# Kernel tuning notes

Measured on AMD Instinct MI355X. Metric: run time of the kernel, lower is better.

Reference implementation:

```python
import jax, jax.numpy as jnp
import numpy as np

V, E, L = 32000, 512, 2  # vocab_size, n_embd (== hidden), n_layer
B, T = 8, 1024


def setup_inputs() -> dict:
    key = jax.random.key(0)
    ks = jax.random.split(key, 6)
    inp = jax.random.randint(ks[0], (B, T), 0, V)
    wte = jax.random.normal(ks[1], (V, E), dtype=jnp.float32) * 0.02
    # PyTorch LSTM params per layer: weight_ih [4H, in], weight_hh [4H, H], b_ih [4H], b_hh [4H]
    W_ih = jax.random.normal(ks[2], (L, 4 * E, E), dtype=jnp.float32) * 0.04
    W_hh = jax.random.normal(ks[3], (L, 4 * E, E), dtype=jnp.float32) * 0.04
    b_ih = jnp.zeros((L, 4 * E), dtype=jnp.float32)
    b_hh = jnp.zeros((L, 4 * E), dtype=jnp.float32)
    fc_w = jax.random.normal(ks[4], (V, E), dtype=jnp.float32) * 0.02
    fc_b = jnp.zeros((V,), dtype=jnp.float32)
    return {"inp": inp, "wte": wte, "W_ih": W_ih, "W_hh": W_hh,
            "b_ih": b_ih, "b_hh": b_hh, "fc_w": fc_w, "fc_b": fc_b}


def _lstm_stack(x, W_ih, W_hh, b_ih, b_hh):
    # x: [B, T, E]; multi-layer LSTM, zero initial (h, c), PyTorch gate order i,f,g,o
    H = W_hh.shape[-1]
    n_layers = W_ih.shape[0]
    for l in range(n_layers):
        # input-to-hidden part is time-parallel: precompute once per layer
        xg = jnp.einsum('bte,ge->btg', x, W_ih[l]) + b_ih[l] + b_hh[l]  # [B,T,4H]
        Whh = W_hh[l]
        h0 = jnp.zeros((x.shape[0], H), x.dtype)
        c0 = jnp.zeros((x.shape[0], H), x.dtype)

        def step(carry, xg_t, Whh=Whh):
            h, c = carry
            g = xg_t + h @ Whh.T  # [B,4H]
            i, f, gg, o = jnp.split(g, 4, axis=-1)
            c = jax.nn.sigmoid(f) * c + jax.nn.sigmoid(i) * jnp.tanh(gg)
            h = jax.nn.sigmoid(o) * jnp.tanh(c)
            return (h, c), h

        (_, _), hs = jax.lax.scan(step, (h0, c0), jnp.swapaxes(xg, 0, 1))  # hs: [T,B,H]
        x = jnp.swapaxes(hs, 0, 1)  # [B,T,H] feeds next layer
    return x


def reference(inp, wte, W_ih, W_hh, b_ih, b_hh, fc_w, fc_b):
    x = wte[inp]  # [B,T,E] embedding lookup
    h = _lstm_stack(x, W_ih, W_hh, b_ih, b_hh)  # [B,T,H]
    logits = jnp.einsum('bth,vh->btv', h, fc_w) + fc_b  # [B,T,V]
    return logits
```

## Files before the change

### kernel.cpp

```cpp
#include <hip/hip_runtime.h>
#include <stdint.h>

typedef __attribute__((ext_vector_type(4))) float f32x4;
typedef __attribute__((ext_vector_type(8))) short s16x8;
typedef __attribute__((ext_vector_type(4))) unsigned short u16x4;
typedef __attribute__((ext_vector_type(4))) unsigned int u32x4;

#define T_SEQ 1024
#define HID 512

__device__ __forceinline__ unsigned short f2bf(float f) {
  uint32_t u = __float_as_uint(f);
  u += 0x7fffu + ((u >> 16) & 1u);
  return (unsigned short)(u >> 16);
}
__device__ __forceinline__ float sigf(float x) { return 1.f / (1.f + __expf(-x)); }
__device__ __forceinline__ float tanhfast(float x) {
  float e = __expf(2.f * x);
  return (e - 1.f) / (e + 1.f);
}

#define ASTORE(p, v) __hip_atomic_store((p), (v), __ATOMIC_RELAXED, __HIP_MEMORY_SCOPE_AGENT)

__device__ __forceinline__ u32x4 load_coh16(const unsigned int* p) {
  u32x4 r;
  asm volatile("global_load_dwordx4 %0, %1, off sc0 sc1" : "=v"(r) : "v"(p) : "memory");
  return r;
}
#define VM_WAIT0 do { asm volatile("s_waitcnt vmcnt(0)" ::: "memory"); \
                      __builtin_amdgcn_sched_barrier(0); } while (0)

#define GLL(gp, lp)                                                      \
  __builtin_amdgcn_global_load_lds(                                     \
      (const __attribute__((address_space(1))) void*)(gp),              \
      (__attribute__((address_space(3))) void*)(lp), 16, 0, 0)

__global__ __launch_bounds__(256) void embed_kernel(const int* __restrict__ inp,
                                                    const float* __restrict__ wte,
                                                    unsigned short* __restrict__ xbf) {
  const int m = blockIdx.x;
  const int idx = inp[m];
  const float* src = wte + (size_t)idx * HID;
  unsigned short* dst = xbf + (size_t)m * HID;
  const int e = threadIdx.x;
  dst[e] = f2bf(src[e]);
  dst[e + 256] = f2bf(src[e + 256]);
}

__global__ __launch_bounds__(256) void cvt_bf16_kernel(const float* __restrict__ src,
                                                       unsigned short* __restrict__ dst,
                                                       int n4) {
  const int i = blockIdx.x * 256 + threadIdx.x;
  if (i >= n4) return;
  f32x4 v = ((const f32x4*)src)[i];
  u16x4 o;
  o.x = f2bf(v.x); o.y = f2bf(v.y); o.z = f2bf(v.z); o.w = f2bf(v.w);
  ((u16x4*)dst)[i] = o;
}

__global__ __launch_bounds__(256) void bias_sum_kernel(const float* __restrict__ a,
                                                       const float* __restrict__ b,
                                                       float* __restrict__ o, int n) {
  const int i = blockIdx.x * 256 + threadIdx.x;
  if (i < n) o[i] = a[i] + b[i];
}

template <int MODE>
__global__ __launch_bounds__(256) void gemm_bt(const unsigned short* __restrict__ A,
                                               const unsigned short* __restrict__ B,
                                               float* __restrict__ C,
                                               const float* __restrict__ bias,
                                               int M, int N, int K) {
  __shared__ unsigned short As[128 * 32];
  __shared__ unsigned short Bs[128 * 32];
  const int nTiles = N >> 7;
  const int mt = blockIdx.x / nTiles;
  const int nt = blockIdx.x - mt * nTiles;
  const int m0 = mt << 7, n0 = nt << 7;
  const int tid = threadIdx.x;
  const int wave = tid >> 6, lane = tid & 63;
  const int wm = wave >> 1, wn = wave & 1;

  const int c1 = wave * 64 + lane;
  const int c2 = 256 + c1;
  const unsigned short* gA1 = A + (size_t)(m0 + (c1 >> 2)) * K + (c1 & 3) * 8;
  const unsigned short* gA2 = A + (size_t)(m0 + (c2 >> 2)) * K + (c2 & 3) * 8;
  const unsigned short* gB1 = B + (size_t)(n0 + (c1 >> 2)) * K + (c1 & 3) * 8;
  const unsigned short* gB2 = B + (size_t)(n0 + (c2 >> 2)) * K + (c2 & 3) * 8;
  unsigned short* lA1 = As + wave * 512;
  unsigned short* lA2 = As + 2048 + wave * 512;
  unsigned short* lB1 = Bs + wave * 512;
  unsigned short* lB2 = Bs + 2048 + wave * 512;

  f32x4 acc[4][4] = {};
  const int row_lo = lane & 15;
  const int kq = (lane >> 4) * 8;

  for (int k0 = 0; k0 < K; k0 += 32) {
    GLL(gA1 + k0, lA1);
    GLL(gA2 + k0, lA2);
    GLL(gB1 + k0, lB1);
    GLL(gB2 + k0, lB2);
    __syncthreads();
    s16x8 af[4], bfr[4];
#pragma unroll
    for (int f = 0; f < 4; ++f) {
      af[f] = *(const s16x8*)(As + (wm * 64 + f * 16 + row_lo) * 32 + kq);
      bfr[f] = *(const s16x8*)(Bs + (wn * 64 + f * 16 + row_lo) * 32 + kq);
    }
#pragma unroll
    for (int i = 0; i < 4; ++i)
#pragma unroll
      for (int j = 0; j < 4; ++j)
        acc[i][j] = __builtin_amdgcn_mfma_f32_16x16x32_bf16(af[i], bfr[j], acc[i][j], 0, 0, 0);
    __syncthreads();
  }

  float bv[4];
#pragma unroll
  for (int j = 0; j < 4; ++j) bv[j] = bias[n0 + wn * 64 + j * 16 + row_lo];
  const int rbase = (lane >> 4) * 4;
#pragma unroll
  for (int i = 0; i < 4; ++i) {
#pragma unroll
    for (int r = 0; r < 4; ++r) {
      const int m = m0 + wm * 64 + i * 16 + rbase + r;
      const size_t row = MODE == 1 ? ((size_t)(m & 7) * T_SEQ + (m >> 3))
                       : MODE == 2 ? ((size_t)(m & (T_SEQ - 1)) * 8 + (m >> 10))
                                   : (size_t)m;
      float* cp = C + row * (size_t)N;
#pragma unroll
      for (int j = 0; j < 4; ++j) cp[n0 + wn * 64 + j * 16 + row_lo] = acc[i][j][r] + bv[j];
    }
  }
}

template <bool IS_L1>
__device__ __forceinline__ void lstm_side(
    int wg, int tid,
    const float* __restrict__ xg1t,
    const unsigned short* __restrict__ Wa,
    const unsigned short* __restrict__ Wb,
    const float* __restrict__ bias2,
    unsigned int* __restrict__ h1T,
    unsigned int* __restrict__ h2T,
    unsigned short* __restrict__ h2out,
    char* hlds, float* GT) {
  constexpr int NKT = IS_L1 ? 16 : 32;
  constexpr int RB = IS_L1 ? 1024 : 2048;
  const int g = tid >> 6, l = tid & 63;
  const int unit = l & 15, grp = l >> 4;
  const int u0 = wg * 16;
  const int row = l & 7;

  s16x8 bfr[NKT];
  {
    const size_t grow = (size_t)(g * 512 + u0 + unit) * 512;
#pragma unroll
    for (int kt = 0; kt < NKT; ++kt) {
      const unsigned short* W = (IS_L1 || kt < 16) ? Wa : Wb;
      bfr[kt] = *(const s16x8*)(W + grow + (kt & 15) * 32 + grp * 8);
    }
  }

  const int sr = tid & 7, sc = tid >> 3;
  const int sb0 = (sr * RB + sc * 32) ^ (sr << 4);
  const int sb1 = (sr * RB + sc * 32 + 16) ^ (sr << 4);
  const int sb2 = (sr * RB + 1024 + sc * 32) ^ (sr << 4);
  const int sb3 = (sr * RB + 1024 + sc * 32 + 16) ^ (sr << 4);

  const int pb = l & 7, pu = l >> 3;
  float bias_g[2][4];
  if constexpr (!IS_L1) {
    if (g == 0) {
#pragma unroll
      for (int r = 0; r < 2; ++r)
#pragma unroll
        for (int gg = 0; gg < 4; ++gg)
          bias_g[r][gg] = bias2[gg * 512 + u0 + r * 8 + pu];
    }
  }
  float cst0 = 0.f, cst1 = 0.f;

  for (int t = 0; t < T_SEQ; ++t) {
    float xv[2][4];
    if constexpr (IS_L1) {
      if (g == 0) {
#pragma unroll
        for (int r = 0; r < 2; ++r)
#pragma unroll
          for (int gg = 0; gg < 4; ++gg)
            xv[r][gg] = xg1t[(size_t)(t * 8 + pb) * 2048 + gg * 512 + u0 + r * 8 + pu];
      }
    }

    if constexpr (IS_L1) {
      u32x4 w0 = {}, w1 = {};
      if (t > 0) {
        const unsigned int* src = h1T + (size_t)(t - 1) * 4096 + sr * 512 + sc * 16;
        const unsigned int tg = (unsigned int)t;
        u32x4 d0, d1, d2, d3;
        for (;;) {
          d0 = load_coh16(src); d1 = load_coh16(src + 4);
          d2 = load_coh16(src + 8); d3 = load_coh16(src + 12);
          VM_WAIT0;
          bool ok = true;
#pragma unroll
          for (int j = 0; j < 4; ++j) {
            ok &= (d0[j] >> 16) == tg; ok &= (d1[j] >> 16) == tg;
            ok &= (d2[j] >> 16) == tg; ok &= (d3[j] >> 16) == tg;
          }
          if (__ballot(ok) == ~0ULL) break;
          __builtin_amdgcn_s_sleep(1);
        }
        w0 = u32x4{(d0[0] & 0xffffu) | (d0[1] << 16), (d0[2] & 0xffffu) | (d0[3] << 16),
                   (d1[0] & 0xffffu) | (d1[1] << 16), (d1[2] & 0xffffu) | (d1[3] << 16)};
        w1 = u32x4{(d2[0] & 0xffffu) | (d2[1] << 16), (d2[2] & 0xffffu) | (d2[3] << 16),
                   (d3[0] & 0xffffu) | (d3[1] << 16), (d3[2] & 0xffffu) | (d3[3] << 16)};
      }
      *(u32x4*)(hlds + sb0) = w0;
      *(u32x4*)(hlds + sb1) = w1;
    } else {
      const unsigned int* src1 = h1T + (size_t)t * 4096 + sr * 512 + sc * 16;
      const unsigned int tg1 = (unsigned int)(t + 1);
      u32x4 d0, d1, d2, d3, e0 = {}, e1 = {}, e2 = {}, e3 = {};
      if (t > 0) {
        const unsigned int* src2 = h2T + (size_t)(t - 1) * 4096 + sr * 512 + sc * 16;
        const unsigned int tg2 = (unsigned int)t;
        for (;;) {
          d0 = load_coh16(src1); d1 = load_coh16(src1 + 4);
          d2 = load_coh16(src1 + 8); d3 = load_coh16(src1 + 12);
          e0 = load_coh16(src2); e1 = load_coh16(src2 + 4);
          e2 = load_coh16(src2 + 8); e3 = load_coh16(src2 + 12);
          VM_WAIT0;
          bool ok = true;
#pragma unroll
          for (int j = 0; j < 4; ++j) {
            ok &= (d0[j] >> 16) == tg1; ok &= (d1[j] >> 16) == tg1;
            ok &= (d2[j] >> 16) == tg1; ok &= (d3[j] >> 16) == tg1;
            ok &= (e0[j] >> 16) == tg2; ok &= (e1[j] >> 16) == tg2;
            ok &= (e2[j] >> 16) == tg2; ok &= (e3[j] >> 16) == tg2;
          }
          if (__ballot(ok) == ~0ULL) break;
          __builtin_amdgcn_s_sleep(1);
        }
      } else {
        for (;;) {
          d0 = load_coh16(src1); d1 = load_coh16(src1 + 4);
          d2 = load_coh16(src1 + 8); d3 = load_coh16(src1 + 12);
          VM_WAIT0;
          bool ok = true;
#pragma unroll
          for (int j = 0; j < 4; ++j) {
            ok &= (d0[j] >> 16) == tg1; ok &= (d1[j] >> 16) == tg1;
            ok &= (d2[j] >> 16) == tg1; ok &= (d3[j] >> 16) == tg1;
          }
          if (__ballot(ok) == ~0ULL) break;
          __builtin_amdgcn_s_sleep(1);
        }
      }
      *(u32x4*)(hlds + sb0) =
          u32x4{(d0[0] & 0xffffu) | (d0[1] << 16), (d0[2] & 0xffffu) | (d0[3] << 16),
                (d1[0] & 0xffffu) | (d1[1] << 16), (d1[2] & 0xffffu) | (d1[3] << 16)};
      *(u32x4*)(hlds + sb1) =
          u32x4{(d2[0] & 0xffffu) | (d2[1] << 16), (d2[2] & 0xffffu) | (d2[3] << 16),
                (d3[0] & 0xffffu) | (d3[1] << 16), (d3[2] & 0xffffu) | (d3[3] << 16)};
      *(u32x4*)(hlds + sb2) =
          u32x4{(e0[0] & 0xffffu) | (e0[1] << 16), (e0[2] & 0xffffu) | (e0[3] << 16),
                (e1[0] & 0xffffu) | (e1[1] << 16), (e1[2] & 0xffffu) | (e1[3] << 16)};
      *(u32x4*)(hlds + sb3) =
          u32x4{(e2[0] & 0xffffu) | (e2[1] << 16), (e2[2] & 0xffffu) | (e2[3] << 16),
                (e3[0] & 0xffffu) | (e3[1] << 16), (e3[2] & 0xffffu) | (e3[3] << 16)};
    }
    __syncthreads();

    f32x4 a0 = {}, a1 = {}, a2 = {}, a3 = {};
#pragma unroll
    for (int kt = 0; kt < NKT; kt += 4) {
      s16x8 x0 = *(const s16x8*)(hlds + ((row * RB + (kt + 0) * 64 + grp * 16) ^ (row << 4)));
      s16x8 x1 = *(const s16x8*)(hlds + ((row * RB + (kt + 1) * 64 + grp * 16) ^ (row << 4)));
      s16x8 x2 = *(const s16x8*)(hlds + ((row * RB + (kt + 2) * 64 + grp * 16) ^ (row << 4)));
      s16x8 x3 = *(const s16x8*)(hlds + ((row * RB + (kt + 3) * 64 + grp * 16) ^ (row << 4)));
      a0 = __builtin_amdgcn_mfma_f32_16x16x32_bf16(x0, bfr[kt + 0], a0, 0, 0, 0);
      a1 = __builtin_amdgcn_mfma_f32_16x16x32_bf16(x1, bfr[kt + 1], a1, 0, 0, 0);
      a2 = __builtin_amdgcn_mfma_f32_16x16x32_bf16(x2, bfr[kt + 2], a2, 0, 0, 0);
      a3 = __builtin_amdgcn_mfma_f32_16x16x32_bf16(x3, bfr[kt + 3], a3, 0, 0, 0);
    }
    f32x4 acc = (a0 + a1) + (a2 + a3);

    if (grp < 2) *(f32x4*)(GT + g * 128 + unit * 8 + grp * 4) = acc;
    __syncthreads();

    if (g == 0) {
      const unsigned int tago = (unsigned int)(t + 1) << 16;
#pragma unroll
      for (int r = 0; r < 2; ++r) {
        const int u = r * 8 + pu;
        float gi = GT[0 + u * 8 + pb];
        float gf = GT[128 + u * 8 + pb];
        float gg = GT[256 + u * 8 + pb];
        float go = GT[384 + u * 8 + pb];
        if constexpr (IS_L1) {
          gi += xv[r][0]; gf += xv[r][1]; gg += xv[r][2]; go += xv[r][3];
        } else {
          gi += bias_g[r][0]; gf += bias_g[r][1]; gg += bias_g[r][2]; go += bias_g[r][3];
        }
        float& cc = r ? cst1 : cst0;
        cc = sigf(gf) * cc + sigf(gi) * tanhfast(gg);
        const float hv = sigf(go) * tanhfast(cc);
        const unsigned int hb16 = f2bf(hv);
        unsigned int* hT = IS_L1 ? h1T : h2T;
        ASTORE(hT + (size_t)t * 4096 + pb * 512 + u0 + u, hb16 | tago);
        if constexpr (!IS_L1)
          h2out[(size_t)(t * 8 + pb) * 512 + u0 + u] = (unsigned short)hb16;
      }
    }
  }
}

__global__ __launch_bounds__(256, 1) void lstm_kernel(
    const float* __restrict__ xg1t,
    const unsigned short* __restrict__ whh1,
    const unsigned short* __restrict__ wih2,
    const unsigned short* __restrict__ whh2,
    const float* __restrict__ bias2,
    unsigned int* __restrict__ h1T, unsigned int* __restrict__ h2T,
    unsigned short* __restrict__ h2out) {
  __shared__ __align__(16) char hlds[16384];
  __shared__ float GT[512];
  const int wg = blockIdx.x, tid = threadIdx.x;
  if (wg < 32)
    lstm_side<true>(wg, tid, xg1t, whh1, nullptr, nullptr, h1T, h2T, h2out, hlds, GT);
  else
    lstm_side<false>(wg - 32, tid, xg1t, wih2, whh2, bias2, h1T, h2T, h2out, hlds, GT);
}

extern "C" void kernel_launch(void* const* d_in, const int* in_sizes, int n_in,
                              void* d_out, int out_size, void* d_ws, size_t ws_size,
                              hipStream_t stream) {
  (void)in_sizes; (void)n_in; (void)out_size; (void)ws_size;
  const int* inp = (const int*)d_in[0];
  const float* wte = (const float*)d_in[1];
  const float* W_ih = (const float*)d_in[2];
  const float* W_hh = (const float*)d_in[3];
  const float* b_ih = (const float*)d_in[4];
  const float* b_hh = (const float*)d_in[5];
  const float* fc_w = (const float*)d_in[6];
  const float* fc_b = (const float*)d_in[7];
  float* out = (float*)d_out;

  char* ob = (char*)d_out;
  float* xg1t = (float*)(ob);
  unsigned int* h1T = (unsigned int*)(ob + (64u << 20));
  unsigned int* h2T = (unsigned int*)(ob + (80u << 20));
  unsigned short* x_bf = (unsigned short*)(ob + (96u << 20));
  unsigned short* whh_bf = (unsigned short*)(ob + (104u << 20));
  unsigned short* wih_bf = (unsigned short*)(ob + (108u << 20));

  char* ws = (char*)d_ws;
  unsigned short* fcw_bf = (unsigned short*)(ws);
  float* bias12 = (float*)(ws + (32u << 20));
  unsigned short* h2bf = (unsigned short*)(ws + (35u << 20));

  hipMemsetAsync(ob + (64u << 20), 0, 32u << 20, stream);
  embed_kernel<<<8192, 256, 0, stream>>>(inp, wte, x_bf);
  cvt_bf16_kernel<<<2048, 256, 0, stream>>>(W_ih, wih_bf, 2 * 2048 * 512 / 4);
  cvt_bf16_kernel<<<2048, 256, 0, stream>>>(W_hh, whh_bf, 2 * 2048 * 512 / 4);
  cvt_bf16_kernel<<<16000, 256, 0, stream>>>(fc_w, fcw_bf, 32000 * 512 / 4);
  bias_sum_kernel<<<16, 256, 0, stream>>>(b_ih, b_hh, bias12, 4096);
  gemm_bt<2><<<64 * 16, 256, 0, stream>>>(x_bf, wih_bf, xg1t, bias12, 8192, 2048, 512);
  lstm_kernel<<<64, 256, 0, stream>>>(xg1t, whh_bf, wih_bf + (size_t)2048 * 512,
                                      whh_bf + (size_t)2048 * 512, bias12 + 2048,
                                      h1T, h2T, h2bf);
  gemm_bt<1><<<64 * 250, 256, 0, stream>>>(h2bf, fcw_bf, out, fc_b, 8192, 32000, 512);
}
```

Baseline: 4.935 ms.

## Fuse both LSTM layers into one 32-workgroup wavefront-pipelined kernel

Replaces the split design, where 32 workgroups ran layer 1 and 32 ran layer 2, with one kernel in which each of 32 workgroups computes a 16-unit slice of both layers. Layer 2 runs two steps behind layer 1 and reads a double-buffered layer-1 hidden state. The xg1 GEMM output goes back to row-major order, so the transposed store mode is dropped. Each group now holds all three weight slices in registers and does more serial work per step. In exchange the per-step flag polls cover both layers in one loop, and the spin loop has a bounded iteration cap that could fall through without valid data.

```diff
diff --git a/kernel.cpp b/kernel.cpp
--- a/kernel.cpp
+++ b/kernel.cpp
@@ -21,6 +21,7 @@
 }
 
 #define ASTORE(p, v) __hip_atomic_store((p), (v), __ATOMIC_RELAXED, __HIP_MEMORY_SCOPE_AGENT)
+#define MFMA(a, b, c) __builtin_amdgcn_mfma_f32_16x16x32_bf16((a), (b), (c), 0, 0, 0)
 
 __device__ __forceinline__ u32x4 load_coh16(const unsigned int* p) {
   u32x4 r;
@@ -112,7 +113,7 @@
     for (int i = 0; i < 4; ++i)
 #pragma unroll
       for (int j = 0; j < 4; ++j)
-        acc[i][j] = __builtin_amdgcn_mfma_f32_16x16x32_bf16(af[i], bfr[j], acc[i][j], 0, 0, 0);
+        acc[i][j] = MFMA(af[i], bfr[j], acc[i][j]);
     __syncthreads();
   }
 
@@ -125,9 +126,7 @@
 #pragma unroll
     for (int r = 0; r < 4; ++r) {
       const int m = m0 + wm * 64 + i * 16 + rbase + r;
-      const size_t row = MODE == 1 ? ((size_t)(m & 7) * T_SEQ + (m >> 3))
-                       : MODE == 2 ? ((size_t)(m & (T_SEQ - 1)) * 8 + (m >> 10))
-                                   : (size_t)m;
+      const size_t row = MODE == 1 ? ((size_t)(m & 7) * T_SEQ + (m >> 3)) : (size_t)m;
       float* cp = C + row * (size_t)N;
 #pragma unroll
       for (int j = 0; j < 4; ++j) cp[n0 + wn * 64 + j * 16 + row_lo] = acc[i][j][r] + bv[j];
@@ -135,204 +134,214 @@
   }
 }
 
-template <bool IS_L1>
-__device__ __forceinline__ void lstm_side(
-    int wg, int tid,
-    const float* __restrict__ xg1t,
-    const unsigned short* __restrict__ Wa,
-    const unsigned short* __restrict__ Wb,
+__global__ __launch_bounds__(256, 1) void lstm_fused(
+    const float* __restrict__ xg1,
+    const unsigned short* __restrict__ whh1,
+    const unsigned short* __restrict__ wih2,
+    const unsigned short* __restrict__ whh2,
     const float* __restrict__ bias2,
     unsigned int* __restrict__ h1T,
     unsigned int* __restrict__ h2T,
-    unsigned short* __restrict__ h2out,
-    char* hlds, float* GT) {
-  constexpr int NKT = IS_L1 ? 16 : 32;
-  constexpr int RB = IS_L1 ? 1024 : 2048;
+    unsigned short* __restrict__ h2out) {
+  __shared__ __align__(16) char lds1[2][8192];
+  __shared__ __align__(16) char lds2[8192];
+  __shared__ float GT1[512];
+  __shared__ float GT2[512];
+
+  const int tid = threadIdx.x;
+  const int wg = blockIdx.x;
   const int g = tid >> 6, l = tid & 63;
   const int unit = l & 15, grp = l >> 4;
   const int u0 = wg * 16;
   const int row = l & 7;
 
-  s16x8 bfr[NKT];
+  s16x8 b1[16], b2i[16], b2h[16];
   {
     const size_t grow = (size_t)(g * 512 + u0 + unit) * 512;
 #pragma unroll
-    for (int kt = 0; kt < NKT; ++kt) {
-      const unsigned short* W = (IS_L1 || kt < 16) ? Wa : Wb;
-      bfr[kt] = *(const s16x8*)(W + grow + (kt & 15) * 32 + grp * 8);
-    }
-  }
-
-  const int sr = tid & 7, sc = tid >> 3;
-  const int sb0 = (sr * RB + sc * 32) ^ (sr << 4);
-  const int sb1 = (sr * RB + sc * 32 + 16) ^ (sr << 4);
-  const int sb2 = (sr * RB + 1024 + sc * 32) ^ (sr << 4);
-  const int sb3 = (sr * RB + 1024 + sc * 32 + 16) ^ (sr << 4);
+    for (int kt = 0; kt < 16; ++kt) {
+      b1[kt] = *(const s16x8*)(whh1 + grow + kt * 32 + grp * 8);
+      b2i[kt] = *(const s16x8*)(wih2 + grow + kt * 32 + grp * 8);
+      b2h[kt] = *(const s16x8*)(whh2 + grow + kt * 32 + grp * 8);
+    }
+  }
 
   const int pb = l & 7, pu = l >> 3;
   float bias_g[2][4];
-  if constexpr (!IS_L1) {
-    if (g == 0) {
+  if (g == 0) {
+#pragma unroll
+    for (int r = 0; r < 2; ++r)
+#pragma unroll
+      for (int gg = 0; gg < 4; ++gg)
+        bias_g[r][gg] = bias2[gg * 512 + u0 + r * 8 + pu];
+  }
+  float c1a = 0.f, c1b = 0.f, c2a = 0.f, c2b = 0.f;
+
+  const int sr = tid & 7, sc = tid >> 3;
+  const int so0 = (sr * 1024 + sc * 32) ^ (sr << 4);
+  const int so1 = (sr * 1024 + sc * 32 + 16) ^ (sr << 4);
+  const int srcoff = sr * 512 + sc * 16;
+
+  for (int t = 0; t <= T_SEQ + 1; ++t) {
+    const int cur = t & 1;
+
+    float xv[2][4];
+    if (g == 0 && t < T_SEQ) {
 #pragma unroll
       for (int r = 0; r < 2; ++r)
 #pragma unroll
         for (int gg = 0; gg < 4; ++gg)
-          bias_g[r][gg] = bias2[gg * 512 + u0 + r * 8 + pu];
-    }
-  }
-  float cst0 = 0.f, cst1 = 0.f;
-
-  for (int t = 0; t < T_SEQ; ++t) {
-    float xv[2][4];
-    if constexpr (IS_L1) {
-      if (g == 0) {
-#pragma unroll
-        for (int r = 0; r < 2; ++r)
-#pragma unroll
-          for (int gg = 0; gg < 4; ++gg)
-            xv[r][gg] = xg1t[(size_t)(t * 8 + pb) * 2048 + gg * 512 + u0 + r * 8 + pu];
-      }
-    }
-
-    if constexpr (IS_L1) {
-      u32x4 w0 = {}, w1 = {};
-      if (t > 0) {
-        const unsigned int* src = h1T + (size_t)(t - 1) * 4096 + sr * 512 + sc * 16;
-        const unsigned int tg = (unsigned int)t;
-        u32x4 d0, d1, d2, d3;
-        for (;;) {
-          d0 = load_coh16(src); d1 = load_coh16(src + 4);
-          d2 = load_coh16(src + 8); d3 = load_coh16(src + 12);
-          VM_WAIT0;
-          bool ok = true;
-#pragma unroll
-          for (int j = 0; j < 4; ++j) {
-            ok &= (d0[j] >> 16) == tg; ok &= (d1[j] >> 16) == tg;
-            ok &= (d2[j] >> 16) == tg; ok &= (d3[j] >> 16) == tg;
-          }
-          if (__ballot(ok) == ~0ULL) break;
-          __builtin_amdgcn_s_sleep(1);
+          xv[r][gg] = xg1[((size_t)pb * T_SEQ + t) * 2048 + gg * 512 + u0 + r * 8 + pu];
+    }
+
+    const bool need1 = (t >= 1) && (t <= T_SEQ);
+    const bool need2 = (t >= 3);
+    if (need1 || need2) {
+      const unsigned int* s1 = h1T + (size_t)(t - 1) * 4096 + srcoff;
+      const unsigned int* s2 = h2T + (size_t)(t - 3) * 4096 + srcoff;
+      const unsigned int tg1 = (unsigned int)t, tg2 = (unsigned int)(t - 2);
+      u32x4 d0 = {}, d1 = {}, d2 = {}, d3 = {}, e0 = {}, e1 = {}, e2 = {}, e3 = {};
+      int spin = 0;
+      for (;;) {
+        if (need1) {
+          d0 = load_coh16(s1); d1 = load_coh16(s1 + 4);
+          d2 = load_coh16(s1 + 8); d3 = load_coh16(s1 + 12);
         }
-        w0 = u32x4{(d0[0] & 0xffffu) | (d0[1] << 16), (d0[2] & 0xffffu) | (d0[3] << 16),
-                   (d1[0] & 0xffffu) | (d1[1] << 16), (d1[2] & 0xffffu) | (d1[3] << 16)};
-        w1 = u32x4{(d2[0] & 0xffffu) | (d2[1] << 16), (d2[2] & 0xffffu) | (d2[3] << 16),
-                   (d3[0] & 0xffffu) | (d3[1] << 16), (d3[2] & 0xffffu) | (d3[3] << 16)};
-      }
-      *(u32x4*)(hlds + sb0) = w0;
-      *(u32x4*)(hlds + sb1) = w1;
-    } else {
-      const unsigned int* src1 = h1T + (size_t)t * 4096 + sr * 512 + sc * 16;
-      const unsigned int tg1 = (unsigned int)(t + 1);
-      u32x4 d0, d1, d2, d3, e0 = {}, e1 = {}, e2 = {}, e3 = {};
-      if (t > 0) {
-        const unsigned int* src2 = h2T + (size_t)(t - 1) * 4096 + sr * 512 + sc * 16;
-        const unsigned int tg2 = (unsigned int)t;
-        for (;;) {
-          d0 = load_coh16(src1); d1 = load_coh16(src1 + 4);
-          d2 = load_coh16(src1 + 8); d3 = load_coh16(src1 + 12);
-          e0 = load_coh16(src2); e1 = load_coh16(src2 + 4);
-          e2 = load_coh16(src2 + 8); e3 = load_coh16(src2 + 12);
-          VM_WAIT0;
-          bool ok = true;
-#pragma unroll
-          for (int j = 0; j < 4; ++j) {
-            ok &= (d0[j] >> 16) == tg1; ok &= (d1[j] >> 16) == tg1;
-            ok &= (d2[j] >> 16) == tg1; ok &= (d3[j] >> 16) == tg1;
-            ok &= (e0[j] >> 16) == tg2; ok &= (e1[j] >> 16) == tg2;
-            ok &= (e2[j] >> 16) == tg2; ok &= (e3[j] >> 16) == tg2;
-          }
-          if (__ballot(ok) == ~0ULL) break;
-          __builtin_amdgcn_s_sleep(1);
+        if (need2) {
+          e0 = load_coh16(s2); e1 = load_coh16(s2 + 4);
+          e2 = load_coh16(s2 + 8); e3 = load_coh16(s2 + 12);
         }
-      } else {
-        for (;;) {
-          d0 = load_coh16(src1); d1 = load_coh16(src1 + 4);
-          d2 = load_coh16(src1 + 8); d3 = load_coh16(src1 + 12);
-          VM_WAIT0;
-          bool ok = true;
+        VM_WAIT0;
+        bool ok = true;
+        if (need1) {
 #pragma unroll
           for (int j = 0; j < 4; ++j) {
             ok &= (d0[j] >> 16) == tg1; ok &= (d1[j] >> 16) == tg1;
             ok &= (d2[j] >> 16) == tg1; ok &= (d3[j] >> 16) == tg1;
           }
-          if (__ballot(ok) == ~0ULL) break;
-          __builtin_amdgcn_s_sleep(1);
         }
-      }
-      *(u32x4*)(hlds + sb0) =
-          u32x4{(d0[0] & 0xffffu) | (d0[1] << 16), (d0[2] & 0xffffu) | (d0[3] << 16),
-                (d1[0] & 0xffffu) | (d1[1] << 16), (d1[2] & 0xffffu) | (d1[3] << 16)};
-      *(u32x4*)(hlds + sb1) =
-          u32x4{(d2[0] & 0xffffu) | (d2[1] << 16), (d2[2] & 0xffffu) | (d2[3] << 16),
-                (d3[0] & 0xffffu) | (d3[1] << 16), (d3[2] & 0xffffu) | (d3[3] << 16)};
-      *(u32x4*)(hlds + sb2) =
-          u32x4{(e0[0] & 0xffffu) | (e0[1] << 16), (e0[2] & 0xffffu) | (e0[3] << 16),
-                (e1[0] & 0xffffu) | (e1[1] << 16), (e1[2] & 0xffffu) | (e1[3] << 16)};
-      *(u32x4*)(hlds + sb3) =
-          u32x4{(e2[0] & 0xffffu) | (e2[1] << 16), (e2[2] & 0xffffu) | (e2[3] << 16),
-                (e3[0] & 0xffffu) | (e3[1] << 16), (e3[2] & 0xffffu) | (e3[3] << 16)};
-    }
-    __syncthreads();
-
-    f32x4 a0 = {}, a1 = {}, a2 = {}, a3 = {};
-#pragma unroll
-    for (int kt = 0; kt < NKT; kt += 4) {
-      s16x8 x0 = *(const s16x8*)(hlds + ((row * RB + (kt + 0) * 64 + grp * 16) ^ (row << 4)));
-      s16x8 x1 = *(const s16x8*)(hlds + ((row * RB + (kt + 1) * 64 + grp * 16) ^ (row << 4)));
-      s16x8 x2 = *(const s16x8*)(hlds + ((row * RB + (kt + 2) * 64 + grp * 16) ^ (row << 4)));
-      s16x8 x3 = *(const s16x8*)(hlds + ((row * RB + (kt + 3) * 64 + grp * 16) ^ (row << 4)));
-      a0 = __builtin_amdgcn_mfma_f32_16x16x32_bf16(x0, bfr[kt + 0], a0, 0, 0, 0);
-      a1 = __builtin_amdgcn_mfma_f32_16x16x32_bf16(x1, bfr[kt + 1], a1, 0, 0, 0);
-      a2 = __builtin_amdgcn_mfma_f32_16x16x32_bf16(x2, bfr[kt + 2], a2, 0, 0, 0);
-      a3 = __builtin_amdgcn_mfma_f32_16x16x32_bf16(x3, bfr[kt + 3], a3, 0, 0, 0);
-    }
-    f32x4 acc = (a0 + a1) + (a2 + a3);
-
-    if (grp < 2) *(f32x4*)(GT + g * 128 + unit * 8 + grp * 4) = acc;
-    __syncthreads();
-
-    if (g == 0) {
-      const unsigned int tago = (unsigned int)(t + 1) << 16;
+        if (need2) {
+#pragma unroll
+          for (int j = 0; j < 4; ++j) {
+            ok &= (e0[j] >> 16) == tg2; ok &= (e1[j] >> 16) == tg2;
+            ok &= (e2[j] >> 16) == tg2; ok &= (e3[j] >> 16) == tg2;
+          }
+        }
+        if (__ballot(ok) == ~0ULL) break;
+        if (++spin > (1 << 14)) break;
+        __builtin_amdgcn_s_sleep(1);
+      }
+      if (need1) {
+        *(u32x4*)(lds1[cur] + so0) =
+            u32x4{(d0[0] & 0xffffu) | (d0[1] << 16), (d0[2] & 0xffffu) | (d0[3] << 16),
+                  (d1[0] & 0xffffu) | (d1[1] << 16), (d1[2] & 0xffffu) | (d1[3] << 16)};
+        *(u32x4*)(lds1[cur] + so1) =
+            u32x4{(d2[0] & 0xffffu) | (d2[1] << 16), (d2[2] & 0xffffu) | (d2[3] << 16),
+                  (d3[0] & 0xffffu) | (d3[1] << 16), (d3[2] & 0xffffu) | (d3[3] << 16)};
+      }
+      if (need2) {
+        *(u32x4*)(lds2 + so0) =
+            u32x4{(e0[0] & 0xffffu) | (e0[1] << 16), (e0[2] & 0xffffu) | (e0[3] << 16),
+                  (e1[0] & 0xffffu) | (e1[1] << 16), (e1[2] & 0xffffu) | (e1[3] << 16)};
+        *(u32x4*)(lds2 + so1) =
+            u32x4{(e2[0] & 0xffffu) | (e2[1] << 16), (e2[2] & 0xffffu) | (e2[3] << 16),
+                  (e3[0] & 0xffffu) | (e3[1] << 16), (e3[2] & 0xffffu) | (e3[3] << 16)};
+      }
+    }
+    if (t == 0) {
+      *(u32x4*)(lds1[0] + so0) = u32x4{0, 0, 0, 0};
+      *(u32x4*)(lds1[0] + so1) = u32x4{0, 0, 0, 0};
+    }
+    if (t == 2) {
+      *(u32x4*)(lds2 + so0) = u32x4{0, 0, 0, 0};
+      *(u32x4*)(lds2 + so1) = u32x4{0, 0, 0, 0};
+    }
+    __syncthreads();
+
+    if (t < T_SEQ) {
+      const char* hb = lds1[cur];
+      f32x4 q0 = {}, q1 = {}, q2 = {}, q3 = {};
+#pragma unroll
+      for (int kt = 0; kt < 16; kt += 4) {
+        s16x8 x0 = *(const s16x8*)(hb + ((row * 1024 + (kt + 0) * 64 + grp * 16) ^ (row << 4)));
+        s16x8 x1 = *(const s16x8*)(hb + ((row * 1024 + (kt + 1) * 64 + grp * 16) ^ (row << 4)));
+        s16x8 x2 = *(const s16x8*)(hb + ((row * 1024 + (kt + 2) * 64 + grp * 16) ^ (row << 4)));
+        s16x8 x3 = *(const s16x8*)(hb + ((row * 1024 + (kt + 3) * 64 + grp * 16) ^ (row << 4)));
+        q0 = MFMA(x0, b1[kt + 0], q0);
+        q1 = MFMA(x1, b1[kt + 1], q1);
+        q2 = MFMA(x2, b1[kt + 2], q2);
+        q3 = MFMA(x3, b1[kt + 3], q3);
+      }
+      f32x4 acc = (q0 + q1) + (q2 + q3);
+      if (grp < 2) *(f32x4*)(GT1 + g * 128 + unit * 8 + grp * 4) = acc;
+    }
+    __syncthreads();
+
+    if (g == 0 && t < T_SEQ) {
 #pragma unroll
       for (int r = 0; r < 2; ++r) {
         const int u = r * 8 + pu;
-        float gi = GT[0 + u * 8 + pb];
-        float gf = GT[128 + u * 8 + pb];
-        float gg = GT[256 + u * 8 + pb];
-        float go = GT[384 + u * 8 + pb];
-        if constexpr (IS_L1) {
-          gi += xv[r][0]; gf += xv[r][1]; gg += xv[r][2]; go += xv[r][3];
-        } else {
-          gi += bias_g[r][0]; gf += bias_g[r][1]; gg += bias_g[r][2]; go += bias_g[r][3];
-        }
-        float& cc = r ? cst1 : cst0;
-        cc = sigf(gf) * cc + sigf(gi) * tanhfast(gg);
+        float gi = GT1[0 + u * 8 + pb] + xv[r][0];
+        float gf = GT1[128 + u * 8 + pb] + xv[r][1];
+        float gv = GT1[256 + u * 8 + pb] + xv[r][2];
+        float go = GT1[384 + u * 8 + pb] + xv[r][3];
+        float& cc = r ? c1b : c1a;
+        cc = sigf(gf) * cc + sigf(gi) * tanhfast(gv);
+        const float hv = sigf(go) * tanhfast(cc);
+        ASTORE(h1T + (size_t)t * 4096 + pb * 512 + u0 + u,
+               (unsigned int)f2bf(hv) | ((unsigned int)(t + 1) << 16));
+      }
+    }
+
+    if (t >= 2) {
+      const char* ha = lds1[cur ^ 1];
+      f32x4 q0 = {}, q1 = {}, q2 = {}, q3 = {};
+#pragma unroll
+      for (int kt = 0; kt < 16; kt += 4) {
+        s16x8 x0 = *(const s16x8*)(ha + ((row * 1024 + (kt + 0) * 64 + grp * 16) ^ (row << 4)));
+        s16x8 x1 = *(const s16x8*)(ha + ((row * 1024 + (kt + 1) * 64 + grp * 16) ^ (row << 4)));
+        s16x8 x2 = *(const s16x8*)(ha + ((row * 1024 + (kt + 2) * 64 + grp * 16) ^ (row << 4)));
+        s16x8 x3 = *(const s16x8*)(ha + ((row * 1024 + (kt + 3) * 64 + grp * 16) ^ (row << 4)));
+        q0 = MFMA(x0, b2i[kt + 0], q0);
+        q1 = MFMA(x1, b2i[kt + 1], q1);
+        q2 = MFMA(x2, b2i[kt + 2], q2);
+        q3 = MFMA(x3, b2i[kt + 3], q3);
+      }
+#pragma unroll
+      for (int kt = 0; kt < 16; kt += 4) {
+        s16x8 x0 = *(const s16x8*)(lds2 + ((row * 1024 + (kt + 0) * 64 + grp * 16) ^ (row << 4)));
+        s16x8 x1 = *(const s16x8*)(lds2 + ((row * 1024 + (kt + 1) * 64 + grp * 16) ^ (row << 4)));
+        s16x8 x2 = *(const s16x8*)(lds2 + ((row * 1024 + (kt + 2) * 64 + grp * 16) ^ (row << 4)));
+        s16x8 x3 = *(const s16x8*)(lds2 + ((row * 1024 + (kt + 3) * 64 + grp * 16) ^ (row << 4)));
+        q0 = MFMA(x0, b2h[kt + 0], q0);
+        q1 = MFMA(x1, b2h[kt + 1], q1);
+        q2 = MFMA(x2, b2h[kt + 2], q2);
+        q3 = MFMA(x3, b2h[kt + 3], q3);
+      }
+      f32x4 acc = (q0 + q1) + (q2 + q3);
+      if (grp < 2) *(f32x4*)(GT2 + g * 128 + unit * 8 + grp * 4) = acc;
+    }
+    __syncthreads();
+
+    if (g == 0 && t >= 2) {
+      const int s = t - 2;
+#pragma unroll
+      for (int r = 0; r < 2; ++r) {
+        const int u = r * 8 + pu;
+        float gi = GT2[0 + u * 8 + pb] + bias_g[r][0];
+        float gf = GT2[128 + u * 8 + pb] + bias_g[r][1];
+        float gv = GT2[256 + u * 8 + pb] + bias_g[r][2];
+        float go = GT2[384 + u * 8 + pb] + bias_g[r][3];
+        float& cc = r ? c2b : c2a;
+        cc = sigf(gf) * cc + sigf(gi) * tanhfast(gv);
         const float hv = sigf(go) * tanhfast(cc);
         const unsigned int hb16 = f2bf(hv);
-        unsigned int* hT = IS_L1 ? h1T : h2T;
-        ASTORE(hT + (size_t)t * 4096 + pb * 512 + u0 + u, hb16 | tago);
-        if constexpr (!IS_L1)
-          h2out[(size_t)(t * 8 + pb) * 512 + u0 + u] = (unsigned short)hb16;
-      }
-    }
-  }
-}
-
-__global__ __launch_bounds__(256, 1) void lstm_kernel(
-    const float* __restrict__ xg1t,
-    const unsigned short* __restrict__ whh1,
-    const unsigned short* __restrict__ wih2,
-    const unsigned short* __restrict__ whh2,
-    const float* __restrict__ bias2,
-    unsigned int* __restrict__ h1T, unsigned int* __restrict__ h2T,
-    unsigned short* __restrict__ h2out) {
-  __shared__ __align__(16) char hlds[16384];
-  __shared__ float GT[512];
-  const int wg = blockIdx.x, tid = threadIdx.x;
-  if (wg < 32)
-    lstm_side<true>(wg, tid, xg1t, whh1, nullptr, nullptr, h1T, h2T, h2out, hlds, GT);
-  else
-    lstm_side<false>(wg - 32, tid, xg1t, wih2, whh2, bias2, h1T, h2T, h2out, hlds, GT);
+        ASTORE(h2T + (size_t)s * 4096 + pb * 512 + u0 + u,
+               hb16 | ((unsigned int)(s + 1) << 16));
+        h2out[((size_t)s * 8 + pb) * 512 + u0 + u] = (unsigned short)hb16;
+      }
+    }
+  }
 }
 
 extern "C" void kernel_launch(void* const* d_in, const int* in_sizes, int n_in,
@@ -350,7 +359,7 @@
   float* out = (float*)d_out;
 
   char* ob = (char*)d_out;
-  float* xg1t = (float*)(ob);
+  float* xg1 = (float*)(ob);
   unsigned int* h1T = (unsigned int*)(ob + (64u << 20));
   unsigned int* h2T = (unsigned int*)(ob + (80u << 20));
   unsigned short* x_bf = (unsigned short*)(ob + (96u << 20));
@@ -368,9 +377,9 @@
   cvt_bf16_kernel<<<2048, 256, 0, stream>>>(W_hh, whh_bf, 2 * 2048 * 512 / 4);
   cvt_bf16_kernel<<<16000, 256, 0, stream>>>(fc_w, fcw_bf, 32000 * 512 / 4);
   bias_sum_kernel<<<16, 256, 0, stream>>>(b_ih, b_hh, bias12, 4096);
-  gemm_bt<2><<<64 * 16, 256, 0, stream>>>(x_bf, wih_bf, xg1t, bias12, 8192, 2048, 512);
-  lstm_kernel<<<64, 256, 0, stream>>>(xg1t, whh_bf, wih_bf + (size_t)2048 * 512,
-                                      whh_bf + (size_t)2048 * 512, bias12 + 2048,
-                                      h1T, h2T, h2bf);
+  gemm_bt<0><<<64 * 16, 256, 0, stream>>>(x_bf, wih_bf, xg1, bias12, 8192, 2048, 512);
+  lstm_fused<<<32, 256, 0, stream>>>(xg1, whh_bf, wih_bf + (size_t)2048 * 512,
+                                     whh_bf + (size_t)2048 * 512, bias12 + 2048,
+                                     h1T, h2T, h2bf);
   gemm_bt<1><<<64 * 250, 256, 0, stream>>>(h2bf, fcw_bf, out, fc_b, 8192, 32000, 512);
 }
```

Result: slower. 6.147 ms (+24.6%).
